# Kernel optimization log

Measured on AMD Instinct MI355X. Metric: run time of the kernel, lower is better.

The kernel has to match this reference:

```python
import jax, jax.numpy as jnp
import numpy as np

VOCAB, D = 32000, 128
B, R, C, T = 8, 100, 64, 32


def setup_inputs() -> dict:
    key = jax.random.key(0)
    k1, k2, k3 = jax.random.split(key, 3)
    x = jax.random.randint(k1, (B, R, C, T), 0, VOCAB, dtype=jnp.int32)
    W_embed = jax.random.normal(k2, (VOCAB, D), dtype=jnp.float32)
    w_pred = jax.random.normal(k3, (1, D), dtype=jnp.float32) * (1.0 / np.sqrt(D))
    b_pred = jnp.zeros((1,), dtype=jnp.float32)
    return {"x": x, "W_embed": W_embed, "w_pred": w_pred, "b_pred": b_pred}


def reference(x, W_embed, w_pred, b_pred):
    # Embedding gather for every cell token at once: [B,R,C,T,D]
    emb = W_embed[x]
    # Mean over tokens within each cell: [B,R,C,D]
    pooled = emb.mean(axis=-2)
    # Dropout is identity in eval mode. Exact (erf) GELU as in torch nn.GELU default.
    act = jax.nn.gelu(pooled, approximate=False)
    # Linear(D -> 1), squeeze to scalar per cell: [B,R,C]
    out = jnp.einsum('brcd,d->brc', act, w_pred[0]) + b_pred[0]
    return out
```

## Files before the change

### kernel.cpp

```cpp
#include <hip/hip_runtime.h>
#include <hip/hip_bf16.h>
#include <math.h>
#include <string.h>

constexpr int VOCAB  = 32000;
constexpr int D      = 128;
constexpr int T      = 32;
constexpr int NCELLS = 8 * 100 * 64;
constexpr int NCHUNK = 2;
constexpr int CDIM   = D / NCHUNK;
constexpr int CHUNK_ELEMS2 = VOCAB * (CDIM / 2);

__device__ inline ushort f2bf(float f) {
    uint32_t u;
    memcpy(&u, &f, 4);
    u += 0x7FFFu + ((u >> 16) & 1u);
    return (ushort)(u >> 16);
}

__device__ inline float gelu_fast(float xv) {
    const float is2 = 0.70710678118654752440f;
    float y  = xv * is2;
    float av = fabsf(y);
    float t  = __builtin_amdgcn_rcpf(__builtin_fmaf(0.3275911f, av, 1.0f));
    float p  = 0.254829592f + t * (-0.284496736f + t * (1.421413741f
             + t * (-1.453152027f + t * 1.061405429f)));
    float e  = __expf(-av * av);
    float er = 1.0f - p * t * e;
    er = copysignf(er, y);
    return 0.5f * xv * (1.0f + er);
}

__global__ __launch_bounds__(256) void convert_W_kernel(
    const float* __restrict__ W, ushort* __restrict__ Wb, float* __restrict__ out)
{
    const int i = blockIdx.x * blockDim.x + threadIdx.x;
    const int v = i >> 5;
    const int k = i & 31;
    const int chunk = k >> 4;
    const int sub   = k & 15;

    float4 src = reinterpret_cast<const float4*>(W)[i];
    ushort4 o;
    o.x = f2bf(src.x); o.y = f2bf(src.y); o.z = f2bf(src.z); o.w = f2bf(src.w);
    reinterpret_cast<ushort4*>(Wb)[(size_t)chunk * (VOCAB * 16) + (size_t)v * 16 + sub] = o;

    if (i < NCELLS) out[i] = 0.0f;
}

__global__ __launch_bounds__(256) void gather_kernel(
    const int*    __restrict__ x,
    const ushort* __restrict__ Wb,
    const float*  __restrict__ w_pred,
    const float*  __restrict__ b_pred,
    float*        __restrict__ out)
{
    const int wave = threadIdx.x >> 6;
    const int lane = threadIdx.x & 63;

    const int slot  = blockIdx.x & 7;
    const int chunk = slot >> 2;
    const int sub   = slot & 3;
    const int g     = blockIdx.x >> 3;
    const int cell  = ((g << 2) + sub) * 4 + wave;

    const int j    = lane & 31;
    const int half = lane >> 5;

    int myidx  = __builtin_nontemporal_load(x + (size_t)cell * T + j);
    int rowoff = myidx << 5;

    const __hip_bfloat162* __restrict__ tbl =
        reinterpret_cast<const __hip_bfloat162*>(Wb) + (size_t)chunk * CHUNK_ELEMS2;

    float ax = 0.0f, ay = 0.0f;
    #pragma unroll
    for (int i = 0; i < T / 2; ++i) {
        int e = __shfl(rowoff, 2 * i + half, 64);
        __hip_bfloat162 v = tbl[(uint32_t)(e + j)];
        float2 f = __bfloat1622float2(v);
        ax += f.x;
        ay += f.y;
    }
    ax += __shfl_xor(ax, 32, 64);
    ay += __shfl_xor(ay, 32, 64);

    float p = (half ? ay : ax) * (1.0f / (float)T);
    float gl = gelu_fast(p);
    float wv = w_pred[chunk * CDIM + 2 * j + half];
    float s = gl * wv;

    #pragma unroll
    for (int off = 32; off >= 1; off >>= 1)
        s += __shfl_xor(s, off, 64);

    if (lane == 0) {
        if (chunk == 0) s += b_pred[0];
        atomicAdd(&out[cell], s);
    }
}

extern "C" void kernel_launch(void* const* d_in, const int* in_sizes, int n_in,
                              void* d_out, int out_size, void* d_ws, size_t ws_size,
                              hipStream_t stream) {
    const int*   x      = (const int*)  d_in[0];
    const float* W      = (const float*)d_in[1];
    const float* w_pred = (const float*)d_in[2];
    const float* b_pred = (const float*)d_in[3];
    float*       out    = (float*)d_out;
    ushort*      Wb     = (ushort*)d_ws;

    const int conv_groups = VOCAB * D / 4;
    convert_W_kernel<<<conv_groups / 256, 256, 0, stream>>>(W, Wb, out);

    gather_kernel<<<NCHUNK * (NCELLS / 4), 256, 0, stream>>>(x, Wb, w_pred, b_pred, out);
}
```

Baseline: 106.2 us.

## Split bf16 table into four 32-dim chunks with 8-byte per-lane gathers

Reorganizes the bf16 embedding table into four column chunks of 32 dims. Each lane now loads a uint2 (four bf16 values) per row, and a wave covers 8 tokens per iteration instead of 2. Partial sums are combined with a transpose-style shuffle reduction. The aim is fewer, wider gather instructions and a smaller per-chunk working set that fits better in cache, at the cost of more blocks, more atomics per cell, and a more complex lane-to-dimension mapping.

```diff
diff --git a/kernel.cpp b/kernel.cpp
--- a/kernel.cpp
+++ b/kernel.cpp
@@ -7,15 +7,21 @@
 constexpr int D      = 128;
 constexpr int T      = 32;
 constexpr int NCELLS = 8 * 100 * 64;
-constexpr int NCHUNK = 2;
+constexpr int NCHUNK = 4;
 constexpr int CDIM   = D / NCHUNK;
-constexpr int CHUNK_ELEMS2 = VOCAB * (CDIM / 2);
 
 __device__ inline ushort f2bf(float f) {
     uint32_t u;
     memcpy(&u, &f, 4);
     u += 0x7FFFu + ((u >> 16) & 1u);
     return (ushort)(u >> 16);
+}
+
+__device__ inline float bf_lo(uint32_t u) {
+    uint32_t b = u << 16; float f; memcpy(&f, &b, 4); return f;
+}
+__device__ inline float bf_hi(uint32_t u) {
+    uint32_t b = u & 0xFFFF0000u; float f; memcpy(&f, &b, 4); return f;
 }
 
 __device__ inline float gelu_fast(float xv) {
@@ -37,13 +43,13 @@
     const int i = blockIdx.x * blockDim.x + threadIdx.x;
     const int v = i >> 5;
     const int k = i & 31;
-    const int chunk = k >> 4;
-    const int sub   = k & 15;
+    const int chunk = k >> 3;
+    const int sub   = k & 7;
 
     float4 src = reinterpret_cast<const float4*>(W)[i];
     ushort4 o;
     o.x = f2bf(src.x); o.y = f2bf(src.y); o.z = f2bf(src.z); o.w = f2bf(src.w);
-    reinterpret_cast<ushort4*>(Wb)[(size_t)chunk * (VOCAB * 16) + (size_t)v * 16 + sub] = o;
+    reinterpret_cast<ushort4*>(Wb)[((size_t)chunk * VOCAB + v) * 8 + sub] = o;
 
     if (i < NCELLS) out[i] = 0.0f;
 }
@@ -59,39 +65,52 @@
     const int lane = threadIdx.x & 63;
 
     const int slot  = blockIdx.x & 7;
-    const int chunk = slot >> 2;
-    const int sub   = slot & 3;
+    const int chunk = slot >> 1;
+    const int sub   = slot & 1;
     const int g     = blockIdx.x >> 3;
-    const int cell  = ((g << 2) + sub) * 4 + wave;
+    const int cell  = ((g << 1) + sub) * 4 + wave;
 
-    const int j    = lane & 31;
-    const int half = lane >> 5;
+    const int j  = lane & 7;
+    const int q  = lane >> 3;
+    const int q4 = q << 2;
 
-    int myidx  = __builtin_nontemporal_load(x + (size_t)cell * T + j);
-    int rowoff = myidx << 5;
+    int myidx  = __builtin_nontemporal_load(x + (size_t)cell * T + (lane & 31));
+    int rowoff = myidx << 3;
 
-    const __hip_bfloat162* __restrict__ tbl =
-        reinterpret_cast<const __hip_bfloat162*>(Wb) + (size_t)chunk * CHUNK_ELEMS2;
+    const uint2* __restrict__ tbl =
+        reinterpret_cast<const uint2*>(Wb) + (size_t)chunk * (VOCAB * 8);
 
-    float ax = 0.0f, ay = 0.0f;
+    float a0 = 0.0f, a1 = 0.0f, a2 = 0.0f, a3 = 0.0f;
     #pragma unroll
-    for (int i = 0; i < T / 2; ++i) {
-        int e = __shfl(rowoff, 2 * i + half, 64);
-        __hip_bfloat162 v = tbl[(uint32_t)(e + j)];
-        float2 f = __bfloat1622float2(v);
-        ax += f.x;
-        ay += f.y;
+    for (int i = 0; i < T / 8; ++i) {
+        int e = __builtin_amdgcn_ds_bpermute(q4 + (i << 5), rowoff);
+        uint2 v = tbl[(uint32_t)(e + j)];
+        a0 += bf_lo(v.x); a1 += bf_hi(v.x);
+        a2 += bf_lo(v.y); a3 += bf_hi(v.y);
     }
-    ax += __shfl_xor(ax, 32, 64);
-    ay += __shfl_xor(ay, 32, 64);
 
-    float p = (half ? ay : ax) * (1.0f / (float)T);
+    const int qb0 = q & 1;
+    float k0 = qb0 ? a2 : a0;
+    float k1 = qb0 ? a3 : a1;
+    float g0 = qb0 ? a0 : a2;
+    float g1 = qb0 ? a1 : a3;
+    k0 += __shfl_xor(g0, 8, 64);
+    k1 += __shfl_xor(g1, 8, 64);
+
+    const int qb1 = (q >> 1) & 1;
+    float m  = qb1 ? k1 : k0;
+    float gm = qb1 ? k0 : k1;
+    m += __shfl_xor(gm, 16, 64);
+    m += __shfl_xor(m, 32, 64);
+
+    const int d = 4 * j + 2 * qb0 + qb1;
+    float p  = m * (1.0f / (float)T);
     float gl = gelu_fast(p);
-    float wv = w_pred[chunk * CDIM + 2 * j + half];
-    float s = gl * wv;
+    float wv = w_pred[chunk * CDIM + d];
+    float s  = gl * wv;
 
     #pragma unroll
-    for (int off = 32; off >= 1; off >>= 1)
+    for (int off = 16; off >= 1; off >>= 1)
         s += __shfl_xor(s, off, 64);
 
     if (lane == 0) {
```

Measured after the change: 131.5 us. 23.8% more time.

## Process full embedding row per wave, drop column chunking and atomics

Applied to the files above, without the earlier changes.

Removes the two-chunk split of the bf16 table, so each wave handles one cell over all 128 dims. Indices are loaded as uniform scalar loads instead of via shuffles, and each lane reads one 32-bit pair from a 256-byte row. Because each cell now has a single writer, the atomicAdd and the output zeroing are replaced by a direct store. This halves the block count and the index reads, but each gathered row now spans the whole table instead of a half-sized chunk, which may lower cache locality.

```diff
diff --git a/kernel.cpp b/kernel.cpp
--- a/kernel.cpp
+++ b/kernel.cpp
@@ -7,15 +7,19 @@
 constexpr int D      = 128;
 constexpr int T      = 32;
 constexpr int NCELLS = 8 * 100 * 64;
-constexpr int NCHUNK = 2;
-constexpr int CDIM   = D / NCHUNK;
-constexpr int CHUNK_ELEMS2 = VOCAB * (CDIM / 2);
 
 __device__ inline ushort f2bf(float f) {
     uint32_t u;
     memcpy(&u, &f, 4);
     u += 0x7FFFu + ((u >> 16) & 1u);
     return (ushort)(u >> 16);
+}
+
+__device__ inline float bf_lo(uint32_t u) {
+    uint32_t b = u << 16; float f; memcpy(&f, &b, 4); return f;
+}
+__device__ inline float bf_hi(uint32_t u) {
+    uint32_t b = u & 0xFFFF0000u; float f; memcpy(&f, &b, 4); return f;
 }
 
 __device__ inline float gelu_fast(float xv) {
@@ -32,20 +36,13 @@
 }
 
 __global__ __launch_bounds__(256) void convert_W_kernel(
-    const float* __restrict__ W, ushort* __restrict__ Wb, float* __restrict__ out)
+    const float* __restrict__ W, ushort* __restrict__ Wb)
 {
     const int i = blockIdx.x * blockDim.x + threadIdx.x;
-    const int v = i >> 5;
-    const int k = i & 31;
-    const int chunk = k >> 4;
-    const int sub   = k & 15;
-
     float4 src = reinterpret_cast<const float4*>(W)[i];
     ushort4 o;
     o.x = f2bf(src.x); o.y = f2bf(src.y); o.z = f2bf(src.z); o.w = f2bf(src.w);
-    reinterpret_cast<ushort4*>(Wb)[(size_t)chunk * (VOCAB * 16) + (size_t)v * 16 + sub] = o;
-
-    if (i < NCELLS) out[i] = 0.0f;
+    reinterpret_cast<ushort4*>(Wb)[i] = o;
 }
 
 __global__ __launch_bounds__(256) void gather_kernel(
@@ -55,49 +52,40 @@
     const float*  __restrict__ b_pred,
     float*        __restrict__ out)
 {
-    const int wave = threadIdx.x >> 6;
     const int lane = threadIdx.x & 63;
+    const int cell = __builtin_amdgcn_readfirstlane(
+        blockIdx.x * 4 + (threadIdx.x >> 6));
 
-    const int slot  = blockIdx.x & 7;
-    const int chunk = slot >> 2;
-    const int sub   = slot & 3;
-    const int g     = blockIdx.x >> 3;
-    const int cell  = ((g << 2) + sub) * 4 + wave;
+    const int* __restrict__ xc = x + (size_t)cell * T;
 
-    const int j    = lane & 31;
-    const int half = lane >> 5;
+    float ax0 = 0.0f, ay0 = 0.0f, ax1 = 0.0f, ay1 = 0.0f;
+    #pragma unroll
+    for (int t = 0; t < T; t += 2) {
+        int i0 = xc[t];
+        int i1 = xc[t + 1];
+        const uint32_t* r0 = reinterpret_cast<const uint32_t*>(Wb + (size_t)i0 * D);
+        const uint32_t* r1 = reinterpret_cast<const uint32_t*>(Wb + (size_t)i1 * D);
+        uint32_t v0 = r0[lane];
+        uint32_t v1 = r1[lane];
+        ax0 += bf_lo(v0); ay0 += bf_hi(v0);
+        ax1 += bf_lo(v1); ay1 += bf_hi(v1);
+    }
+    float ax = ax0 + ax1;
+    float ay = ay0 + ay1;
 
-    int myidx  = __builtin_nontemporal_load(x + (size_t)cell * T + j);
-    int rowoff = myidx << 5;
+    const float inv_t = 1.0f / (float)T;
+    float g0 = gelu_fast(ax * inv_t);
+    float g1 = gelu_fast(ay * inv_t);
 
-    const __hip_bfloat162* __restrict__ tbl =
-        reinterpret_cast<const __hip_bfloat162*>(Wb) + (size_t)chunk * CHUNK_ELEMS2;
-
-    float ax = 0.0f, ay = 0.0f;
-    #pragma unroll
-    for (int i = 0; i < T / 2; ++i) {
-        int e = __shfl(rowoff, 2 * i + half, 64);
-        __hip_bfloat162 v = tbl[(uint32_t)(e + j)];
-        float2 f = __bfloat1622float2(v);
-        ax += f.x;
-        ay += f.y;
-    }
-    ax += __shfl_xor(ax, 32, 64);
-    ay += __shfl_xor(ay, 32, 64);
-
-    float p = (half ? ay : ax) * (1.0f / (float)T);
-    float gl = gelu_fast(p);
-    float wv = w_pred[chunk * CDIM + 2 * j + half];
-    float s = gl * wv;
+    float2 wv = reinterpret_cast<const float2*>(w_pred)[lane];
+    float s = __builtin_fmaf(g0, wv.x, g1 * wv.y);
 
     #pragma unroll
     for (int off = 32; off >= 1; off >>= 1)
         s += __shfl_xor(s, off, 64);
 
-    if (lane == 0) {
-        if (chunk == 0) s += b_pred[0];
-        atomicAdd(&out[cell], s);
-    }
+    if (lane == 0)
+        out[cell] = s + b_pred[0];
 }
 
 extern "C" void kernel_launch(void* const* d_in, const int* in_sizes, int n_in,
@@ -111,7 +99,7 @@
     ushort*      Wb     = (ushort*)d_ws;
 
     const int conv_groups = VOCAB * D / 4;
-    convert_W_kernel<<<conv_groups / 256, 256, 0, stream>>>(W, Wb, out);
+    convert_W_kernel<<<conv_groups / 256, 256, 0, stream>>>(W, Wb);
 
-    gather_kernel<<<NCHUNK * (NCELLS / 4), 256, 0, stream>>>(x, Wb, w_pred, b_pred, out);
+    gather_kernel<<<NCELLS / 4, 256, 0, stream>>>(x, Wb, w_pred, b_pred, out);
 }
```

Result: no change. 105.1 us (-1.0%).
